# Kernel optimization log

Measured on AMD Instinct MI355X. Metric: run time of the kernel, lower is better.

Reference implementation:

```python
import jax, jax.numpy as jnp
import numpy as np

N, H, D = 1024, 64, 3

def _lin(x, W, b=None):
    y = x @ W.T
    return y if b is None else y + b

def setup_inputs() -> dict:
    key = jax.random.key(0)
    ks = jax.random.split(key, 16)
    def gl(k, o, i):  # glorot-ish linear weight
        lim = (6.0 / (i + o)) ** 0.5
        return jax.random.uniform(k, (o, i), minval=-lim, maxval=lim, dtype=jnp.float32)
    inp = {
        "h": jax.random.normal(ks[0], (N, H), dtype=jnp.float32),
        "x": jax.random.uniform(ks[1], (N, D), dtype=jnp.float32),  # coords in [0, L)
        "L": jnp.float32(1.0),
        # edge MLP: (2H+2) -> H -> H, silu both layers
        "ew1": gl(ks[2], H, 2 * H + 2), "eb1": jnp.zeros((H,), jnp.float32),
        "ew2": gl(ks[3], H, H),         "eb2": jnp.zeros((H,), jnp.float32),
        # node MLP: 2H -> H -> H
        "nw1": gl(ks[4], H, 2 * H),     "nb1": jnp.zeros((H,), jnp.float32),
        "nw2": gl(ks[5], H, H),         "nb2": jnp.zeros((H,), jnp.float32),
        # coord path
        "chw": gl(ks[6], H, H),         "chb": jnp.zeros((H,), jnp.float32),
        "cww": 0.001 * gl(ks[7], 1, H),  # small-init, no bias
        # attention gate
        "aw": gl(ks[8], 1, H),          "ab": jnp.zeros((1,), jnp.float32),
    }
    return inp

COORDS_RANGE = 10.0

def reference(h, x, L, ew1, eb1, ew2, eb2, nw1, nb1, nw2, nb2, chw, chb, cww, aw, ab):
    act = jax.nn.silu
    n, hd = h.shape
    # --- coord2radial: toroidal log map, x_i - x_j wrapped to [-L/2, L/2) ---
    diff = jnp.remainder(x[:, None, :] - x[None, :, :] + 0.5 * L, L) - 0.5 * L  # (N,N,D)
    radial = jnp.sum(diff ** 2, axis=-1, keepdims=True)                          # (N,N,1)
    coord_diff = diff / (jnp.sqrt(radial + 1e-8) + 1.0)                          # (N,N,D)
    # --- edge model: MLP([h_i, h_j, r, r]) decomposed to avoid concat ---
    Wa, Wb = ew1[:, :hd], ew1[:, hd:2 * hd]
    wr = ew1[:, 2 * hd] + ew1[:, 2 * hd + 1]                                     # (H,)
    pre = (h @ Wa.T)[:, None, :] + (h @ Wb.T)[None, :, :] + radial * wr + eb1    # (N,N,H)
    edge = act(act(pre) @ ew2.T + eb2)                                           # (N,N,H)
    att = jax.nn.sigmoid(edge @ aw.T + ab)                                       # (N,N,1)
    edge = edge * att
    # --- coord model ---
    ch = act(edge @ chw.T + chb)                                                 # (N,N,H)
    w = jnp.tanh(ch @ cww.T) * COORDS_RANGE                                      # (N,N,1)
    delta = jnp.sum(coord_diff * w, axis=1)                                      # (N,D)
    x_new = jnp.remainder(x + delta, L)
    # --- node model ---
    agg = jnp.sum(edge, axis=1)                                                  # (N,H)
    pre_n = h @ nw1[:, :hd].T + agg @ nw1[:, hd:].T + nb1
    h_new = h + (act(pre_n) @ nw2.T + nb2)                                       # recurrent
    return (h_new, x_new)
```

## Files before the change

### kernel.cpp

```cpp
#include <hip/hip_runtime.h>

#define Nn 1024

typedef __attribute__((ext_vector_type(8))) short short8v;
typedef __attribute__((ext_vector_type(4))) float floatx4;

__device__ __forceinline__ float frcp(float v)  { return __builtin_amdgcn_rcpf(v); }
__device__ __forceinline__ float fsilu(float v) { return v * frcp(1.0f + __expf(-v)); }
__device__ __forceinline__ float fsig(float v)  { return frcp(1.0f + __expf(-v)); }
__device__ __forceinline__ float ftanh10(float v){ return 10.0f - 20.0f * frcp(__expf(2.0f * v) + 1.0f); }

__device__ __forceinline__ unsigned pkbf(float lo, float hi) {
    unsigned a = __float_as_uint(lo) + 0x8000u;
    unsigned b = __float_as_uint(hi) + 0x8000u;
    return __builtin_amdgcn_perm(b, a, 0x07060302u);
}

union I4S8 { int4 i; short8v s; };

__global__ __launch_bounds__(256) void precompute_kernel(
    const float* __restrict__ h, const float* __restrict__ ew1,
    const float* __restrict__ eb1, const float* __restrict__ nw1,
    const float* __restrict__ nb1, float* __restrict__ ha,
    float* __restrict__ hb, float* __restrict__ hn1)
{
    int t = blockIdx.x * 256 + threadIdx.x;
    int which = t >> 16;
    int rem = t & 65535;
    int i = rem >> 6, o = rem & 63;
    const float* hrow = h + i * 64;
    const float* wrow;
    float acc;
    if (which == 0)      { wrow = ew1 + o * 130;      acc = eb1[o]; }
    else if (which == 1) { wrow = ew1 + o * 130 + 64; acc = 0.0f;   }
    else                 { wrow = nw1 + o * 128;      acc = nb1[o]; }
    #pragma unroll
    for (int k = 0; k < 64; ++k) acc = fmaf(hrow[k], wrow[k], acc);
    if (which == 0)      ha[rem]  = acc;
    else if (which == 1) hb[rem]  = acc;
    else                 hn1[rem] = acc;
}

__global__ __launch_bounds__(256) __attribute__((amdgpu_waves_per_eu(2, 3)))
void edge_mfma_kernel(
    const float* __restrict__ x, const float* __restrict__ Lp,
    const float* __restrict__ ha, const float* __restrict__ hb,
    const float* __restrict__ ew1, const float* __restrict__ ew2,
    const float* __restrict__ eb2, const float* __restrict__ chw,
    const float* __restrict__ chb, const float* __restrict__ aw,
    const float* __restrict__ ab, const float* __restrict__ cww,
    float* __restrict__ agg, float* __restrict__ delta)
{
    __shared__ __align__(16) int4 Wlds[2][2][4][64];
    __shared__ __align__(16) float xs[Nn * 3];
    __shared__ float redagg[4][64];
    __shared__ float sdel[4][3];

    const int tid  = threadIdx.x;
    const int wave = tid >> 6, lane = tid & 63;
    const int lr = lane & 15, g = lane >> 4;
    const int i0 = blockIdx.x;
    const int jbase = wave * 256;
    const int ghi  = g >> 1;
    const int selA = (lr + ((g & 1) << 5)) << 2;
    const int selB = selA + 64;
    const int4* WldsF = &Wlds[0][0][0][0];

    {
        const float4* xsrc = (const float4*)x;
        float4* xdst = (float4*)xs;
        xdst[tid] = xsrc[tid];
        xdst[tid + 256] = xsrc[tid + 256];
        xdst[tid + 512] = xsrc[tid + 512];
    }

    if (wave == 0) {
      #pragma unroll
      for (int kt = 0; kt < 2; ++kt)
        #pragma unroll
        for (int nt = 0; nt < 4; ++nt) {
          int n = nt * 16 + lr;
          int k0 = kt * 32 + g * 8;
          float4 lo = *(const float4*)(ew2 + n * 64 + k0);
          float4 hi = *(const float4*)(ew2 + n * 64 + k0 + 4);
          Wlds[0][kt][nt][lane] = make_int4(
              (int)pkbf(lo.x, lo.y), (int)pkbf(lo.z, lo.w),
              (int)pkbf(hi.x, hi.y), (int)pkbf(hi.z, hi.w));
          lo = *(const float4*)(chw + n * 64 + k0);
          hi = *(const float4*)(chw + n * 64 + k0 + 4);
          Wlds[1][kt][nt][lane] = make_int4(
              (int)pkbf(lo.x, lo.y), (int)pkbf(lo.z, lo.w),
              (int)pkbf(hi.x, hi.y), (int)pkbf(hi.z, hi.w));
        }
    }

    floatx4 ebr[4], awr[4], chbr[4], cwr[4];
    #pragma unroll
    for (int nt = 0; nt < 4; ++nt) {
      int n4 = nt * 16 + (g << 2);
      ebr[nt]  = *(const floatx4*)(eb2 + n4);
      awr[nt]  = *(const floatx4*)(aw  + n4);
      chbr[nt] = *(const floatx4*)(chb + n4);
      cwr[nt]  = *(const floatx4*)(cww + n4);
    }

    floatx4 har[4], wrr[4];
    #pragma unroll
    for (int kt = 0; kt < 2; ++kt)
      #pragma unroll
      for (int h = 0; h < 2; ++h) {
        int k0 = kt * 32 + g * 8 + h * 4;
        har[kt * 2 + h] = *(const floatx4*)(ha + i0 * 64 + k0);
        floatx4 wv;
        #pragma unroll
        for (int e = 0; e < 4; ++e) {
          float2 w2v = *(const float2*)(ew1 + (k0 + e) * 130 + 128);
          wv[e] = w2v.x + w2v.y;
        }
        wrr[kt * 2 + h] = wv;
      }

    const float L = Lp[0], invL = frcp(L);
    const float ab0 = ab[0];

    floatx4 agg4[4];
    #pragma unroll
    for (int nt = 0; nt < 4; ++nt) agg4[nt] = (floatx4){0.f, 0.f, 0.f, 0.f};
    float dp0 = 0.f, dp1 = 0.f, dp2 = 0.f;

    __syncthreads();

    const float xi0 = xs[i0 * 3 + 0], xi1 = xs[i0 * 3 + 1], xi2 = xs[i0 * 3 + 2];

    float4 hpre0, hpre1, hpre2, hpre3;
    {
      const float* hn = hb + (jbase + lr) * 64 + g * 8;
      hpre0 = *(const float4*)(hn);
      hpre1 = *(const float4*)(hn + 4);
      hpre2 = *(const float4*)(hn + 32);
      hpre3 = *(const float4*)(hn + 36);
    }

    for (int jc = 0; jc < 16; ++jc) {
      unsigned lidx = (unsigned)lane;
      asm volatile("" : "+v"(lidx));

      float4 h0 = hpre0, h1 = hpre1, h2 = hpre2, h3 = hpre3;
      if (jc < 15) {
        const float* hn = hb + (jbase + (jc + 1) * 16 + lr) * 64 + g * 8;
        hpre0 = *(const float4*)(hn);
        hpre1 = *(const float4*)(hn + 4);
        hpre2 = *(const float4*)(hn + 32);
        hpre3 = *(const float4*)(hn + 36);
      }

      const int j = jbase + jc * 16 + lr;
      float xd0 = xi0 - xs[j * 3 + 0];
      float xd1 = xi1 - xs[j * 3 + 1];
      float xd2 = xi2 - xs[j * 3 + 2];
      float d0 = xd0 - L * floorf(fmaf(xd0, invL, 0.5f));
      float d1 = xd1 - L * floorf(fmaf(xd1, invL, 0.5f));
      float d2 = xd2 - L * floorf(fmaf(xd2, invL, 0.5f));
      float radial = d0 * d0 + d1 * d1 + d2 * d2;
      float cinv = frcp(__builtin_amdgcn_sqrtf(radial + 1e-8f) + 1.0f);
      float dx0 = d0 * cinv, dx1 = d1 * cinv, dx2 = d2 * cinv;

      short8v tf[2];
      {
        floatx4 p0, p1;
        #pragma unroll
        for (int e = 0; e < 4; ++e) {
          p0[e] = fsilu(fmaf(radial, wrr[0][e], har[0][e]) + h0[e]);
          p1[e] = fsilu(fmaf(radial, wrr[1][e], har[1][e]) + h1[e]);
        }
        union { short8v s; unsigned u[4]; } pk;
        pk.u[0] = pkbf(p0[0], p0[1]); pk.u[1] = pkbf(p0[2], p0[3]);
        pk.u[2] = pkbf(p1[0], p1[1]); pk.u[3] = pkbf(p1[2], p1[3]);
        tf[0] = pk.s;
        #pragma unroll
        for (int e = 0; e < 4; ++e) {
          p0[e] = fsilu(fmaf(radial, wrr[2][e], har[2][e]) + h2[e]);
          p1[e] = fsilu(fmaf(radial, wrr[3][e], har[3][e]) + h3[e]);
        }
        pk.u[0] = pkbf(p0[0], p0[1]); pk.u[1] = pkbf(p0[2], p0[3]);
        pk.u[2] = pkbf(p1[0], p1[1]); pk.u[3] = pkbf(p1[2], p1[3]);
        tf[1] = pk.s;
      }

      floatx4 acc[4];
      #pragma unroll
      for (int nt = 0; nt < 4; ++nt) acc[nt] = ebr[nt];
      #pragma unroll
      for (int kt = 0; kt < 2; ++kt)
        #pragma unroll
        for (int nt = 0; nt < 4; ++nt) {
          I4S8 wv; wv.i = WldsF[(kt * 4 + nt) * 64 + lidx];
          acc[nt] = __builtin_amdgcn_mfma_f32_16x16x32_bf16(wv.s, tf[kt], acc[nt], 0, 0, 0);
        }

      float p = 0.f;
      #pragma unroll
      for (int nt = 0; nt < 4; ++nt)
        #pragma unroll
        for (int r = 0; r < 4; ++r) {
          float s = fsilu(acc[nt][r]);
          acc[nt][r] = s;
          p = fmaf(s, awr[nt][r], p);
        }
      p += __shfl_xor(p, 16); p += __shfl_xor(p, 32);
      const float att = fsig(p + ab0);

      unsigned Pq[4][2];
      #pragma unroll
      for (int nt = 0; nt < 4; ++nt) {
        float e0 = acc[nt][0] * att, e1 = acc[nt][1] * att;
        float e2 = acc[nt][2] * att, e3 = acc[nt][3] * att;
        agg4[nt][0] += e0; agg4[nt][1] += e1;
        agg4[nt][2] += e2; agg4[nt][3] += e3;
        Pq[nt][0] = pkbf(e0, e1);
        Pq[nt][1] = pkbf(e2, e3);
      }

      union { short8v s; int u[4]; } ef[2];
      #pragma unroll
      for (int kt2 = 0; kt2 < 2; ++kt2)
        #pragma unroll
        for (int w = 0; w < 4; ++w) {
          int sel = (w < 2) ? selA : selB;
          int v0 = __builtin_amdgcn_ds_bpermute(sel, (int)Pq[kt2 * 2][w & 1]);
          int v1 = __builtin_amdgcn_ds_bpermute(sel, (int)Pq[kt2 * 2 + 1][w & 1]);
          ef[kt2].u[w] = ghi ? v1 : v0;
        }

      #pragma unroll
      for (int nt = 0; nt < 4; ++nt) acc[nt] = chbr[nt];
      #pragma unroll
      for (int kt2 = 0; kt2 < 2; ++kt2)
        #pragma unroll
        for (int nt = 0; nt < 4; ++nt) {
          I4S8 wv; wv.i = WldsF[512 + (kt2 * 4 + nt) * 64 + lidx];
          acc[nt] = __builtin_amdgcn_mfma_f32_16x16x32_bf16(wv.s, ef[kt2].s, acc[nt], 0, 0, 0);
        }

      float q = 0.f;
      #pragma unroll
      for (int nt = 0; nt < 4; ++nt)
        #pragma unroll
        for (int r = 0; r < 4; ++r)
          q = fmaf(fsilu(acc[nt][r]), cwr[nt][r], q);
      q += __shfl_xor(q, 16); q += __shfl_xor(q, 32);
      const float wvv = ftanh10(q);
      if (g == 0) {
        dp0 = fmaf(dx0, wvv, dp0);
        dp1 = fmaf(dx1, wvv, dp1);
        dp2 = fmaf(dx2, wvv, dp2);
      }
    }

    #pragma unroll
    for (int nt = 0; nt < 4; ++nt)
      #pragma unroll
      for (int r = 0; r < 4; ++r) {
        float v = agg4[nt][r];
        v += __shfl_xor(v, 1); v += __shfl_xor(v, 2);
        v += __shfl_xor(v, 4); v += __shfl_xor(v, 8);
        agg4[nt][r] = v;
      }
    if (lr == 0) {
      #pragma unroll
      for (int nt = 0; nt < 4; ++nt)
        *(floatx4*)&redagg[wave][nt * 16 + (g << 2)] = agg4[nt];
    }
    dp0 += __shfl_xor(dp0, 1); dp0 += __shfl_xor(dp0, 2); dp0 += __shfl_xor(dp0, 4); dp0 += __shfl_xor(dp0, 8);
    dp1 += __shfl_xor(dp1, 1); dp1 += __shfl_xor(dp1, 2); dp1 += __shfl_xor(dp1, 4); dp1 += __shfl_xor(dp1, 8);
    dp2 += __shfl_xor(dp2, 1); dp2 += __shfl_xor(dp2, 2); dp2 += __shfl_xor(dp2, 4); dp2 += __shfl_xor(dp2, 8);
    if (lane == 0) { sdel[wave][0] = dp0; sdel[wave][1] = dp1; sdel[wave][2] = dp2; }
    __syncthreads();
    if (tid < 64)
      agg[i0 * 64 + tid] = redagg[0][tid] + redagg[1][tid] + redagg[2][tid] + redagg[3][tid];
    else if (tid < 67) {
      int d = tid - 64;
      delta[i0 * 3 + d] = sdel[0][d] + sdel[1][d] + sdel[2][d] + sdel[3][d];
    }
}

__global__ __launch_bounds__(256) void node_fused_kernel(
    const float* __restrict__ h, const float* __restrict__ hn1,
    const float* __restrict__ agg, const float* __restrict__ nw1,
    const float* __restrict__ nw2, const float* __restrict__ nb2,
    const float* __restrict__ x, const float* __restrict__ delta,
    const float* __restrict__ Lp, float* __restrict__ outh,
    float* __restrict__ outx)
{
    __shared__ float sps[256];
    const int b = blockIdx.x, tid = threadIdx.x;
    const int gt = b * 256 + tid;
    const int i = gt >> 6, o = gt & 63;
    const float* arow = agg + i * 64;
    const float* wrow = nw1 + o * 128 + 64;
    float acc = hn1[gt];
    #pragma unroll
    for (int k = 0; k < 64; ++k) acc = fmaf(arow[k], wrow[k], acc);
    sps[tid] = fsilu(acc);
    __syncthreads();
    const float* srow = sps + (tid & ~63);
    const float* w2row = nw2 + o * 64;
    float acc2 = h[gt] + nb2[o];
    #pragma unroll
    for (int k = 0; k < 64; ++k) acc2 = fmaf(srow[k], w2row[k], acc2);
    outh[gt] = acc2;
    if (tid < 12) {
        int ii = b * 4 + tid / 3, d = tid % 3;
        float L = Lp[0];
        float v = x[ii * 3 + d] + delta[ii * 3 + d];
        outx[ii * 3 + d] = v - L * floorf(v * frcp(L));
    }
}

extern "C" void kernel_launch(void* const* d_in, const int* in_sizes, int n_in,
                              void* d_out, int out_size, void* d_ws, size_t ws_size,
                              hipStream_t stream) {
    const float* h   = (const float*)d_in[0];
    const float* x   = (const float*)d_in[1];
    const float* Lp  = (const float*)d_in[2];
    const float* ew1 = (const float*)d_in[3];
    const float* eb1 = (const float*)d_in[4];
    const float* ew2 = (const float*)d_in[5];
    const float* eb2 = (const float*)d_in[6];
    const float* nw1 = (const float*)d_in[7];
    const float* nb1 = (const float*)d_in[8];
    const float* nw2 = (const float*)d_in[9];
    const float* nb2 = (const float*)d_in[10];
    const float* chw = (const float*)d_in[11];
    const float* chb = (const float*)d_in[12];
    const float* cww = (const float*)d_in[13];
    const float* aw  = (const float*)d_in[14];
    const float* ab  = (const float*)d_in[15];

    float* ws    = (float*)d_ws;
    float* ha    = ws;
    float* hb    = ws + 65536;
    float* hn1   = ws + 131072;
    float* agg   = ws + 196608;
    float* delta = ws + 262144;

    float* outh = (float*)d_out;
    float* outx = outh + 65536;

    precompute_kernel<<<768, 256, 0, stream>>>(h, ew1, eb1, nw1, nb1, ha, hb, hn1);
    edge_mfma_kernel<<<1024, 256, 0, stream>>>(x, Lp, ha, hb, ew1, ew2, eb2, chw, chb,
                                               aw, ab, cww, agg, delta);
    node_fused_kernel<<<256, 256, 0, stream>>>(h, hn1, agg, nw1, nw2, nb2, x, delta,
                                               Lp, outh, outx);
}
```

Measured before the change: 95.15 us.

## Move per-row constants to LDS, use hardware bf16 pack, raise occupancy

Per-thread register arrays for biases, attention and coordinate weights, ha and the radial weights are replaced by an LDS table that is re-read inside the inner loop. This frees VGPRs so the waves_per_eu hint can be raised from 2-3 to 3-4. The manual round-and-permute bf16 packing is swapped for the v_cvt_pk_bf16_f32 instruction. The cost is extra LDS reads per iteration, and the new conversion may round differently from the old bias-add truncation.

```diff
diff --git a/kernel.cpp b/kernel.cpp
--- a/kernel.cpp
+++ b/kernel.cpp
@@ -10,10 +10,10 @@
 __device__ __forceinline__ float fsig(float v)  { return frcp(1.0f + __expf(-v)); }
 __device__ __forceinline__ float ftanh10(float v){ return 10.0f - 20.0f * frcp(__expf(2.0f * v) + 1.0f); }
 
-__device__ __forceinline__ unsigned pkbf(float lo, float hi) {
-    unsigned a = __float_as_uint(lo) + 0x8000u;
-    unsigned b = __float_as_uint(hi) + 0x8000u;
-    return __builtin_amdgcn_perm(b, a, 0x07060302u);
+__device__ __forceinline__ unsigned cvtpk(float lo, float hi) {
+    unsigned r;
+    asm("v_cvt_pk_bf16_f32 %0, %1, %2" : "=v"(r) : "v"(lo), "v"(hi));
+    return r;
 }
 
 union I4S8 { int4 i; short8v s; };
@@ -41,7 +41,7 @@
     else                 hn1[rem] = acc;
 }
 
-__global__ __launch_bounds__(256) __attribute__((amdgpu_waves_per_eu(2, 3)))
+__global__ __launch_bounds__(256) __attribute__((amdgpu_waves_per_eu(3, 4)))
 void edge_mfma_kernel(
     const float* __restrict__ x, const float* __restrict__ Lp,
     const float* __restrict__ ha, const float* __restrict__ hb,
@@ -51,7 +51,8 @@
     const float* __restrict__ ab, const float* __restrict__ cww,
     float* __restrict__ agg, float* __restrict__ delta)
 {
-    __shared__ __align__(16) int4 Wlds[2][2][4][64];
+    __shared__ __align__(16) int4 Wlds[1024];
+    __shared__ __align__(16) float cvec[384];
     __shared__ __align__(16) float xs[Nn * 3];
     __shared__ float redagg[4][64];
     __shared__ float sdel[4][3];
@@ -64,7 +65,7 @@
     const int ghi  = g >> 1;
     const int selA = (lr + ((g & 1) << 5)) << 2;
     const int selB = selA + 64;
-    const int4* WldsF = &Wlds[0][0][0][0];
+    const int4* WldsF = &Wlds[0];
 
     {
         const float4* xsrc = (const float4*)x;
@@ -83,42 +84,24 @@
           int k0 = kt * 32 + g * 8;
           float4 lo = *(const float4*)(ew2 + n * 64 + k0);
           float4 hi = *(const float4*)(ew2 + n * 64 + k0 + 4);
-          Wlds[0][kt][nt][lane] = make_int4(
-              (int)pkbf(lo.x, lo.y), (int)pkbf(lo.z, lo.w),
-              (int)pkbf(hi.x, hi.y), (int)pkbf(hi.z, hi.w));
+          Wlds[(kt * 4 + nt) * 64 + lane] = make_int4(
+              (int)cvtpk(lo.x, lo.y), (int)cvtpk(lo.z, lo.w),
+              (int)cvtpk(hi.x, hi.y), (int)cvtpk(hi.z, hi.w));
           lo = *(const float4*)(chw + n * 64 + k0);
           hi = *(const float4*)(chw + n * 64 + k0 + 4);
-          Wlds[1][kt][nt][lane] = make_int4(
-              (int)pkbf(lo.x, lo.y), (int)pkbf(lo.z, lo.w),
-              (int)pkbf(hi.x, hi.y), (int)pkbf(hi.z, hi.w));
-        }
-    }
-
-    floatx4 ebr[4], awr[4], chbr[4], cwr[4];
-    #pragma unroll
-    for (int nt = 0; nt < 4; ++nt) {
-      int n4 = nt * 16 + (g << 2);
-      ebr[nt]  = *(const floatx4*)(eb2 + n4);
-      awr[nt]  = *(const floatx4*)(aw  + n4);
-      chbr[nt] = *(const floatx4*)(chb + n4);
-      cwr[nt]  = *(const floatx4*)(cww + n4);
-    }
-
-    floatx4 har[4], wrr[4];
-    #pragma unroll
-    for (int kt = 0; kt < 2; ++kt)
-      #pragma unroll
-      for (int h = 0; h < 2; ++h) {
-        int k0 = kt * 32 + g * 8 + h * 4;
-        har[kt * 2 + h] = *(const floatx4*)(ha + i0 * 64 + k0);
-        floatx4 wv;
-        #pragma unroll
-        for (int e = 0; e < 4; ++e) {
-          float2 w2v = *(const float2*)(ew1 + (k0 + e) * 130 + 128);
-          wv[e] = w2v.x + w2v.y;
-        }
-        wrr[kt * 2 + h] = wv;
-      }
+          Wlds[512 + (kt * 4 + nt) * 64 + lane] = make_int4(
+              (int)cvtpk(lo.x, lo.y), (int)cvtpk(lo.z, lo.w),
+              (int)cvtpk(hi.x, hi.y), (int)cvtpk(hi.z, hi.w));
+        }
+    }
+    if (tid < 64) {
+      cvec[tid]       = eb2[tid];
+      cvec[64 + tid]  = aw[tid];
+      cvec[128 + tid] = chb[tid];
+      cvec[192 + tid] = cww[tid];
+      cvec[256 + tid] = ha[i0 * 64 + tid];
+      cvec[320 + tid] = ew1[tid * 130 + 128] + ew1[tid * 130 + 129];
+    }
 
     const float L = Lp[0], invL = frcp(L);
     const float ab0 = ab[0];
@@ -144,6 +127,12 @@
     for (int jc = 0; jc < 16; ++jc) {
       unsigned lidx = (unsigned)lane;
       asm volatile("" : "+v"(lidx));
+      unsigned cb = (unsigned)(g << 4);
+      asm volatile("" : "+v"(cb));
+      unsigned hbo = (unsigned)(g << 5);
+      asm volatile("" : "+v"(hbo));
+      const float* cvp = (const float*)((const char*)cvec + cb);
+      const float* hvp = (const float*)((const char*)cvec + 1024 + hbo);
 
       float4 h0 = hpre0, h1 = hpre1, h2 = hpre2, h3 = hpre3;
       if (jc < 15) {
@@ -167,29 +156,33 @@
 
       short8v tf[2];
       {
-        floatx4 p0, p1;
-        #pragma unroll
-        for (int e = 0; e < 4; ++e) {
-          p0[e] = fsilu(fmaf(radial, wrr[0][e], har[0][e]) + h0[e]);
-          p1[e] = fsilu(fmaf(radial, wrr[1][e], har[1][e]) + h1[e]);
-        }
         union { short8v s; unsigned u[4]; } pk;
-        pk.u[0] = pkbf(p0[0], p0[1]); pk.u[1] = pkbf(p0[2], p0[3]);
-        pk.u[2] = pkbf(p1[0], p1[1]); pk.u[3] = pkbf(p1[2], p1[3]);
-        tf[0] = pk.s;
-        #pragma unroll
-        for (int e = 0; e < 4; ++e) {
-          p0[e] = fsilu(fmaf(radial, wrr[2][e], har[2][e]) + h2[e]);
-          p1[e] = fsilu(fmaf(radial, wrr[3][e], har[3][e]) + h3[e]);
-        }
-        pk.u[0] = pkbf(p0[0], p0[1]); pk.u[1] = pkbf(p0[2], p0[3]);
-        pk.u[2] = pkbf(p1[0], p1[1]); pk.u[3] = pkbf(p1[2], p1[3]);
-        tf[1] = pk.s;
+        #pragma unroll
+        for (int kt = 0; kt < 2; ++kt) {
+          floatx4 ha0 = *(const floatx4*)(hvp + kt * 32);
+          floatx4 ha1 = *(const floatx4*)(hvp + kt * 32 + 4);
+          floatx4 wr0 = *(const floatx4*)(hvp + 64 + kt * 32);
+          floatx4 wr1 = *(const floatx4*)(hvp + 64 + kt * 32 + 4);
+          const float4& hA = kt ? h2 : h0;
+          const float4& hB = kt ? h3 : h1;
+          floatx4 p0, p1;
+          p0[0] = fsilu(fmaf(radial, wr0[0], ha0[0]) + hA.x);
+          p0[1] = fsilu(fmaf(radial, wr0[1], ha0[1]) + hA.y);
+          p0[2] = fsilu(fmaf(radial, wr0[2], ha0[2]) + hA.z);
+          p0[3] = fsilu(fmaf(radial, wr0[3], ha0[3]) + hA.w);
+          p1[0] = fsilu(fmaf(radial, wr1[0], ha1[0]) + hB.x);
+          p1[1] = fsilu(fmaf(radial, wr1[1], ha1[1]) + hB.y);
+          p1[2] = fsilu(fmaf(radial, wr1[2], ha1[2]) + hB.z);
+          p1[3] = fsilu(fmaf(radial, wr1[3], ha1[3]) + hB.w);
+          pk.u[0] = cvtpk(p0[0], p0[1]); pk.u[1] = cvtpk(p0[2], p0[3]);
+          pk.u[2] = cvtpk(p1[0], p1[1]); pk.u[3] = cvtpk(p1[2], p1[3]);
+          tf[kt] = pk.s;
+        }
       }
 
       floatx4 acc[4];
       #pragma unroll
-      for (int nt = 0; nt < 4; ++nt) acc[nt] = ebr[nt];
+      for (int nt = 0; nt < 4; ++nt) acc[nt] = *(const floatx4*)(cvp + nt * 16);
       #pragma unroll
       for (int kt = 0; kt < 2; ++kt)
         #pragma unroll
@@ -200,13 +193,15 @@
 
       float p = 0.f;
       #pragma unroll
-      for (int nt = 0; nt < 4; ++nt)
+      for (int nt = 0; nt < 4; ++nt) {
+        floatx4 awv = *(const floatx4*)(cvp + 64 + nt * 16);
         #pragma unroll
         for (int r = 0; r < 4; ++r) {
           float s = fsilu(acc[nt][r]);
           acc[nt][r] = s;
-          p = fmaf(s, awr[nt][r], p);
-        }
+          p = fmaf(s, awv[r], p);
+        }
+      }
       p += __shfl_xor(p, 16); p += __shfl_xor(p, 32);
       const float att = fsig(p + ab0);
 
@@ -217,8 +212,8 @@
         float e2 = acc[nt][2] * att, e3 = acc[nt][3] * att;
         agg4[nt][0] += e0; agg4[nt][1] += e1;
         agg4[nt][2] += e2; agg4[nt][3] += e3;
-        Pq[nt][0] = pkbf(e0, e1);
-        Pq[nt][1] = pkbf(e2, e3);
+        Pq[nt][0] = cvtpk(e0, e1);
+        Pq[nt][1] = cvtpk(e2, e3);
       }
 
       union { short8v s; int u[4]; } ef[2];
@@ -233,7 +228,7 @@
         }
 
       #pragma unroll
-      for (int nt = 0; nt < 4; ++nt) acc[nt] = chbr[nt];
+      for (int nt = 0; nt < 4; ++nt) acc[nt] = *(const floatx4*)(cvp + 128 + nt * 16);
       #pragma unroll
       for (int kt2 = 0; kt2 < 2; ++kt2)
         #pragma unroll
@@ -244,10 +239,12 @@
 
       float q = 0.f;
       #pragma unroll
-      for (int nt = 0; nt < 4; ++nt)
+      for (int nt = 0; nt < 4; ++nt) {
+        floatx4 cwv = *(const floatx4*)(cvp + 192 + nt * 16);
         #pragma unroll
         for (int r = 0; r < 4; ++r)
-          q = fmaf(fsilu(acc[nt][r]), cwr[nt][r], q);
+          q = fmaf(fsilu(acc[nt][r]), cwv[r], q);
+      }
       q += __shfl_xor(q, 16); q += __shfl_xor(q, 32);
       const float wvv = ftanh10(q);
       if (g == 0) {
```

Result: no change. 93.31 us (-1.9%).
